# Kernel optimization log

Measured on AMD Instinct MI355X. Metric: run time of the kernel, lower is better.

Reference implementation:

```python
import jax, jax.numpy as jnp
import numpy as np

L = 5          # num_layer
D = 128        # emb_dim
F = 16         # raw node/edge feature dim
N = 50000      # nodes
E = 800000     # edges
BN_EPS = 1e-5


def _bn(z, g, b):
    # BatchNorm1d forward with batch statistics (training-mode math)
    m = z.mean(axis=0)
    v = z.var(axis=0)
    return (z - m) * jax.lax.rsqrt(v + BN_EPS) * g + b


def setup_inputs() -> dict:
    key = jax.random.key(0)
    ks = jax.random.split(key, 8)
    s = lambda *sh: 0.05  # weight scale
    return {
        "x": jax.random.normal(ks[0], (N, F), jnp.float32),
        "edge_index": jax.random.randint(ks[1], (2, E), 0, N, jnp.int32),
        "edge_attr": jax.random.normal(ks[2], (E, F), jnp.float32),
        "W_node": jax.random.normal(ks[3], (F, D), jnp.float32) * 0.05,
        "b_node": jnp.zeros((D,), jnp.float32),
        "We": jax.random.normal(ks[4], (L, F, D), jnp.float32) * 0.05,
        "be": jnp.zeros((L, D), jnp.float32),
        "eps_gin": jnp.zeros((L,), jnp.float32),
        "W1": jax.random.normal(ks[5], (L, D, 2 * D), jnp.float32) * 0.05,
        "b1": jnp.zeros((L, 2 * D), jnp.float32),
        "g1": jnp.ones((L, 2 * D), jnp.float32),
        "beta1": jnp.zeros((L, 2 * D), jnp.float32),
        "W2": jax.random.normal(ks[6], (L, 2 * D, D), jnp.float32) * 0.05,
        "b2": jnp.zeros((L, D), jnp.float32),
        "g_bn": jnp.ones((L, D), jnp.float32),
        "beta_bn": jnp.zeros((L, D), jnp.float32),
    }


def reference(x, edge_index, edge_attr, W_node, b_node, We, be, eps_gin,
              W1, b1, g1, beta1, W2, b2, g_bn, beta_bn):
    src, dst = edge_index[0], edge_index[1]
    n = x.shape[0]
    h = x @ W_node + b_node                       # node encoder: [N, D]
    for l in range(L):
        e = edge_attr @ We[l] + be[l]             # edge encoder: [E, D]
        msg = jax.nn.relu(h[src] + e)             # gather + message
        agg = jax.ops.segment_sum(msg, dst, num_segments=n)  # scatter-add
        z = (1.0 + eps_gin[l]) * h + agg
        z = _bn(z @ W1[l] + b1[l], g1[l], beta1[l])  # GIN MLP hidden
        z = jax.nn.relu(z)
        z = z @ W2[l] + b2[l]                     # GIN MLP out: [N, D]
        z = _bn(z, g_bn[l], beta_bn[l])           # per-layer BatchNorm
        if l < L - 1:
            z = jax.nn.relu(z)                    # dropout is identity (p=0)
        h = z + h                                 # residual
    return h                                      # JK = 'last'
```

## Files before the change

kernel.cpp:

```cpp
#include <hip/hip_runtime.h>
#include <hip/hip_bf16.h>

#define NN 50000
#define EE 800000
#define DD 128
#define FF 16
#define LL 5
#define NB 782

typedef __attribute__((ext_vector_type(8))) short bf16x8;
typedef __attribute__((ext_vector_type(4))) float f32x4;

__device__ __forceinline__ unsigned short f2bf(float f) {
    union { float f; unsigned int u; } v; v.f = f;
    unsigned int u = v.u;
    unsigned int r = (u + 0x7fffu + ((u >> 16) & 1u)) >> 16;
    return (unsigned short)r;
}
__device__ __forceinline__ float bf2f(unsigned short s) {
    union { unsigned int u; float f; } v; v.u = ((unsigned int)s) << 16;
    return v.f;
}
#define BFLO(u) __uint_as_float((unsigned int)(u) << 16)
#define BFHI(u) __uint_as_float((unsigned int)(u) & 0xffff0000u)

__global__ void k_node_enc(const float* __restrict__ x, const float* __restrict__ Wn,
                           const float* __restrict__ bn, float* __restrict__ h,
                           unsigned short* __restrict__ h_bf)
{
    const int t = blockIdx.x * 256 + threadIdx.x;
    const int i = t >> 7, d = t & 127;
    const float4* x4 = (const float4*)(x + (size_t)i * 16);
    float4 a0 = x4[0], a1 = x4[1], a2 = x4[2], a3 = x4[3];
    float acc = bn[d];
    acc += a0.x*Wn[0*128+d] + a0.y*Wn[1*128+d] + a0.z*Wn[2*128+d] + a0.w*Wn[3*128+d];
    acc += a1.x*Wn[4*128+d] + a1.y*Wn[5*128+d] + a1.z*Wn[6*128+d] + a1.w*Wn[7*128+d];
    acc += a2.x*Wn[8*128+d] + a2.y*Wn[9*128+d] + a2.z*Wn[10*128+d] + a2.w*Wn[11*128+d];
    acc += a3.x*Wn[12*128+d] + a3.y*Wn[13*128+d] + a3.z*Wn[14*128+d] + a3.w*Wn[15*128+d];
    h[t] = acc;
    h_bf[t] = f2bf(acc);
}

__global__ void k_count(const int* __restrict__ ei, int* __restrict__ counts)
{
    const int e = blockIdx.x * 256 + threadIdx.x;
    atomicAdd(&counts[ei[EE + e]], 1);
}

__global__ __launch_bounds__(1024) void k_scan(int* __restrict__ counts, int* __restrict__ row_ptr)
{
    __shared__ int wsum[16];
    __shared__ int carry;
    const int tid = threadIdx.x, lane = tid & 63, w = tid >> 6;
    if (tid == 0) carry = 0;
    __syncthreads();
    for (int base = 0; base < NN; base += 1024) {
        const int i = base + tid;
        const int v = (i < NN) ? counts[i] : 0;
        int x = v;
        #pragma unroll
        for (int off = 1; off < 64; off <<= 1) {
            const int t = __shfl_up(x, off);
            if (lane >= off) x += t;
        }
        if (lane == 63) wsum[w] = x;
        __syncthreads();
        int woff = 0, total = 0;
        #pragma unroll
        for (int j = 0; j < 16; ++j) { const int s = wsum[j]; total += s; if (j < w) woff += s; }
        const int ex = carry + woff + x - v;
        if (i < NN) { row_ptr[i] = ex; counts[i] = ex; }
        __syncthreads();
        if (tid == 0) carry += total;
        __syncthreads();
    }
    if (tid == 0) row_ptr[NN] = carry;
}

__global__ void k_fill(const int* __restrict__ ei, const float* __restrict__ ea,
                       int* __restrict__ cursor, int* __restrict__ src_perm,
                       unsigned short* __restrict__ ea_bf)
{
    const int e = blockIdx.x * 256 + threadIdx.x;
    const int dst = ei[EE + e];
    const int p = atomicAdd(&cursor[dst], 1);
    src_perm[p] = ei[e];
    const float4* s4 = (const float4*)(ea + (size_t)e * 16);
    const float4 a0 = s4[0], a1 = s4[1], a2 = s4[2], a3 = s4[3];
    union { bf16x8 v; unsigned short u[8]; } o0, o1;
    o0.u[0]=f2bf(a0.x); o0.u[1]=f2bf(a0.y); o0.u[2]=f2bf(a0.z); o0.u[3]=f2bf(a0.w);
    o0.u[4]=f2bf(a1.x); o0.u[5]=f2bf(a1.y); o0.u[6]=f2bf(a1.z); o0.u[7]=f2bf(a1.w);
    o1.u[0]=f2bf(a2.x); o1.u[1]=f2bf(a2.y); o1.u[2]=f2bf(a2.z); o1.u[3]=f2bf(a2.w);
    o1.u[4]=f2bf(a3.x); o1.u[5]=f2bf(a3.y); o1.u[6]=f2bf(a3.z); o1.u[7]=f2bf(a3.w);
    bf16x8* dp = (bf16x8*)(ea_bf + (size_t)p * 16);
    dp[0] = o0.v; dp[1] = o1.v;
}

__global__ void k_pack(const float* __restrict__ W1, const float* __restrict__ W2,
                       unsigned short* __restrict__ Wp1, unsigned short* __restrict__ Wp2)
{
    int t = blockIdx.x * 256 + threadIdx.x;
    const int total = LL * 32768;
    if (t < total) {
        const int l = t >> 15, r = t & 32767;
        const int j = r & 7, lane = (r >> 3) & 63, kt = (r >> 9) & 3, nt = r >> 11;
        const int k = kt * 32 + (lane >> 4) * 8 + j;
        const int n = nt * 16 + (lane & 15);
        Wp1[t] = f2bf(W1[(size_t)l * 32768 + k * 256 + n]);
    } else {
        t -= total;
        const int l = t >> 15, r = t & 32767;
        const int j = r & 7, lane = (r >> 3) & 63, kt = (r >> 9) & 7, nt = r >> 12;
        const int k = kt * 32 + (lane >> 4) * 8 + j;
        const int n = nt * 16 + (lane & 15);
        Wp2[t] = f2bf(W2[(size_t)l * 32768 + k * 128 + n]);
    }
}

__global__ __launch_bounds__(256) void k_agg(
    const unsigned short* __restrict__ h_bf, const unsigned short* __restrict__ ea_bf,
    const float* __restrict__ We_l, const float* __restrict__ be_l,
    const float* __restrict__ eps_gin, const int l,
    const int* __restrict__ row_ptr, const int* __restrict__ src_perm,
    unsigned short* __restrict__ z_bf)
{
    const int wv = threadIdx.x >> 6;
    const int v  = blockIdx.x * 4 + wv;
    const int lane = threadIdx.x & 63;
    const int c2 = lane * 2;
    float2 w[16];
    #pragma unroll
    for (int f = 0; f < 16; ++f) w[f] = *(const float2*)(We_l + f * 128 + c2);
    const float2 bed = *(const float2*)(be_l + c2);
    const float epsv = 1.0f + eps_gin[l];
    const int kbeg = __builtin_amdgcn_readfirstlane(row_ptr[v]);
    const int kend = __builtin_amdgcn_readfirstlane(row_ptr[v + 1]);
    float2 acc0 = {0.f,0.f}, acc1 = {0.f,0.f}, acc2 = {0.f,0.f}, acc3 = {0.f,0.f};

#define EDGE_DOT(EA, EB, HQ, OUT) do {                                      \
        float ex_ = bed.x, ey_ = bed.y, a_;                                 \
        a_ = BFLO(EA.x); ex_ += a_*w[0].x;  ey_ += a_*w[0].y;               \
        a_ = BFHI(EA.x); ex_ += a_*w[1].x;  ey_ += a_*w[1].y;               \
        a_ = BFLO(EA.y); ex_ += a_*w[2].x;  ey_ += a_*w[2].y;               \
        a_ = BFHI(EA.y); ex_ += a_*w[3].x;  ey_ += a_*w[3].y;               \
        a_ = BFLO(EA.z); ex_ += a_*w[4].x;  ey_ += a_*w[4].y;               \
        a_ = BFHI(EA.z); ex_ += a_*w[5].x;  ey_ += a_*w[5].y;               \
        a_ = BFLO(EA.w); ex_ += a_*w[6].x;  ey_ += a_*w[6].y;               \
        a_ = BFHI(EA.w); ex_ += a_*w[7].x;  ey_ += a_*w[7].y;               \
        a_ = BFLO(EB.x); ex_ += a_*w[8].x;  ey_ += a_*w[8].y;               \
        a_ = BFHI(EB.x); ex_ += a_*w[9].x;  ey_ += a_*w[9].y;               \
        a_ = BFLO(EB.y); ex_ += a_*w[10].x; ey_ += a_*w[10].y;              \
        a_ = BFHI(EB.y); ex_ += a_*w[11].x; ey_ += a_*w[11].y;              \
        a_ = BFLO(EB.z); ex_ += a_*w[12].x; ey_ += a_*w[12].y;              \
        a_ = BFHI(EB.z); ex_ += a_*w[13].x; ey_ += a_*w[13].y;              \
        a_ = BFLO(EB.w); ex_ += a_*w[14].x; ey_ += a_*w[14].y;              \
        a_ = BFHI(EB.w); ex_ += a_*w[15].x; ey_ += a_*w[15].y;              \
        const float mx_ = BFLO(HQ) + ex_, my_ = BFHI(HQ) + ey_;             \
        OUT.x += mx_ > 0.f ? mx_ : 0.f;                                     \
        OUT.y += my_ > 0.f ? my_ : 0.f;                                     \
    } while (0)

    uint4 ce0, ce1, ce2, ce3, ce4, ce5, ce6, ce7;
    unsigned int ch0, ch1, ch2, ch3;
    int vs0, vs1, vs2, vs3;

    int k = kbeg;
    if (k < kend) {
        const int a0 = __builtin_amdgcn_readfirstlane(src_perm[k]);
        const int a1 = __builtin_amdgcn_readfirstlane(src_perm[k + 1]);
        const int a2 = __builtin_amdgcn_readfirstlane(src_perm[k + 2]);
        const int a3 = __builtin_amdgcn_readfirstlane(src_perm[k + 3]);
        ch0 = *(const unsigned int*)(h_bf + (size_t)a0 * 128 + c2);
        ch1 = *(const unsigned int*)(h_bf + (size_t)a1 * 128 + c2);
        ch2 = *(const unsigned int*)(h_bf + (size_t)a2 * 128 + c2);
        ch3 = *(const unsigned int*)(h_bf + (size_t)a3 * 128 + c2);
        const uint4* ep = (const uint4*)(ea_bf + (size_t)k * 16);
        ce0 = ep[0]; ce1 = ep[1]; ce2 = ep[2]; ce3 = ep[3];
        ce4 = ep[4]; ce5 = ep[5]; ce6 = ep[6]; ce7 = ep[7];
        vs0 = src_perm[k + 4]; vs1 = src_perm[k + 5];
        vs2 = src_perm[k + 6]; vs3 = src_perm[k + 7];
    }
    for (; k < kend; k += 4) {
        const int fs0 = src_perm[k + 8],  fs1 = src_perm[k + 9];
        const int fs2 = src_perm[k + 10], fs3 = src_perm[k + 11];
        const int b0 = __builtin_amdgcn_readfirstlane(vs0);
        const int b1 = __builtin_amdgcn_readfirstlane(vs1);
        const int b2 = __builtin_amdgcn_readfirstlane(vs2);
        const int b3 = __builtin_amdgcn_readfirstlane(vs3);
        const unsigned int nh0 = *(const unsigned int*)(h_bf + (size_t)b0 * 128 + c2);
        const unsigned int nh1 = *(const unsigned int*)(h_bf + (size_t)b1 * 128 + c2);
        const unsigned int nh2 = *(const unsigned int*)(h_bf + (size_t)b2 * 128 + c2);
        const unsigned int nh3 = *(const unsigned int*)(h_bf + (size_t)b3 * 128 + c2);
        const uint4* np_ = (const uint4*)(ea_bf + (size_t)(k + 4) * 16);
        const uint4 ne0 = np_[0], ne1 = np_[1], ne2 = np_[2], ne3 = np_[3];
        const uint4 ne4 = np_[4], ne5 = np_[5], ne6 = np_[6], ne7 = np_[7];
        __builtin_amdgcn_sched_barrier(0);
        EDGE_DOT(ce0, ce1, ch0, acc0);
        if (k + 1 < kend) EDGE_DOT(ce2, ce3, ch1, acc1);
        if (k + 2 < kend) EDGE_DOT(ce4, ce5, ch2, acc2);
        if (k + 3 < kend) EDGE_DOT(ce6, ce7, ch3, acc3);
        ce0=ne0; ce1=ne1; ce2=ne2; ce3=ne3; ce4=ne4; ce5=ne5; ce6=ne6; ce7=ne7;
        ch0=nh0; ch1=nh1; ch2=nh2; ch3=nh3;
        vs0=fs0; vs1=fs1; vs2=fs2; vs3=fs3;
    }
#undef EDGE_DOT
    const unsigned int hv = *(const unsigned int*)(h_bf + (size_t)v * 128 + c2);
    const float zx = epsv * BFLO(hv) + ((acc0.x + acc1.x) + (acc2.x + acc3.x));
    const float zy = epsv * BFHI(hv) + ((acc0.y + acc1.y) + (acc2.y + acc3.y));
    const unsigned int zp = (unsigned int)f2bf(zx) | ((unsigned int)f2bf(zy) << 16);
    *(unsigned int*)(z_bf + (size_t)v * 128 + c2) = zp;
}

__global__ __launch_bounds__(256) void k_gemmB(
    const unsigned short* __restrict__ z_bf,
    const unsigned short* __restrict__ Wp,
    unsigned short* __restrict__ t_bf,
    float* __restrict__ ps1, float* __restrict__ pq1)
{
    const int tid = threadIdx.x;
    const int w = tid >> 6, l6 = tid & 63, m = l6 & 15, quad = l6 >> 4;
    const int r0 = blockIdx.x * 64;
    const bf16x8* Wv = (const bf16x8*)Wp;
    bf16x8 b[4][4];
    #pragma unroll
    for (int ct = 0; ct < 4; ++ct)
        #pragma unroll
        for (int kt = 0; kt < 4; ++kt)
            b[ct][kt] = Wv[((w * 4 + ct) * 4 + kt) * 64 + l6];

    const bf16x8 zero8 = {0,0,0,0,0,0,0,0};
    const f32x4 z4 = {0.f, 0.f, 0.f, 0.f};
    float rs_[4] = {0.f,0.f,0.f,0.f}, rq_[4] = {0.f,0.f,0.f,0.f};

    bf16x8 a[4], an[4];
    {
        const int row = r0 + m;
        #pragma unroll
        for (int kt = 0; kt < 4; ++kt)
            a[kt] = (row < NN) ? *(const bf16x8*)(z_bf + (size_t)row * 128 + kt * 32 + quad * 8) : zero8;
    }
    #pragma unroll
    for (int rt = 0; rt < 4; ++rt) {
        if (rt < 3) {
            const int row = r0 + (rt + 1) * 16 + m;
            #pragma unroll
            for (int kt = 0; kt < 4; ++kt)
                an[kt] = (row < NN) ? *(const bf16x8*)(z_bf + (size_t)row * 128 + kt * 32 + quad * 8) : zero8;
        }
        f32x4 acc[4] = {z4, z4, z4, z4};
        #pragma unroll
        for (int kt = 0; kt < 4; ++kt)
            #pragma unroll
            for (int ct = 0; ct < 4; ++ct)
                acc[ct] = __builtin_amdgcn_mfma_f32_16x16x32_bf16(a[kt], b[ct][kt], acc[ct], 0, 0, 0);
        const int rowb = r0 + rt * 16 + quad * 4;
        #pragma unroll
        for (int ct = 0; ct < 4; ++ct) {
            const int col = w * 64 + ct * 16 + m;
            #pragma unroll
            for (int r = 0; r < 4; ++r) {
                const float val = acc[ct][r];
                if (rowb + r < NN) t_bf[(size_t)(rowb + r) * 256 + col] = f2bf(val);
                rs_[ct] += val; rq_[ct] += val * val;
            }
        }
        #pragma unroll
        for (int kt = 0; kt < 4; ++kt) a[kt] = an[kt];
    }
    #pragma unroll
    for (int ct = 0; ct < 4; ++ct) {
        float ss = rs_[ct], sq = rq_[ct];
        ss += __shfl_xor(ss, 16); ss += __shfl_xor(ss, 32);
        sq += __shfl_xor(sq, 16); sq += __shfl_xor(sq, 32);
        if (quad == 0) {
            const int col = w * 64 + ct * 16 + m;
            atomicAdd(&ps1[col], ss);
            atomicAdd(&pq1[col], sq);
        }
    }
}

__global__ __launch_bounds__(256) void k_gemmD(
    const unsigned short* __restrict__ t_bf,
    const float* __restrict__ ps1, const float* __restrict__ pq1,
    const float* __restrict__ g1, const float* __restrict__ be1,
    const unsigned short* __restrict__ Wp,
    unsigned short* __restrict__ vb,
    float* __restrict__ ps2, float* __restrict__ pq2)
{
    __shared__ __align__(16) unsigned short us[64 * 264];
    __shared__ __align__(16) float scf[256], shf[256];
    const int tid = threadIdx.x;
    {
        const float mean = ps1[tid] * (1.0f / NN);
        const float var  = pq1[tid] * (1.0f / NN) - mean * mean;
        const float sc = g1[tid] * rsqrtf(var + 1e-5f);
        scf[tid] = sc;
        shf[tid] = be1[tid] - mean * sc;
    }
    __syncthreads();
    const int r0 = blockIdx.x * 64;
    {
        const int rb = tid >> 5, c0 = (tid & 31) * 8;
        const float4 s0 = *(const float4*)(scf + c0), s1 = *(const float4*)(scf + c0 + 4);
        const float4 b0 = *(const float4*)(shf + c0), b1 = *(const float4*)(shf + c0 + 4);
        const bf16x8 zero = {0,0,0,0,0,0,0,0};
        #pragma unroll
        for (int rr = 0; rr < 8; ++rr) {
            const int row = rr * 8 + rb, g = r0 + row;
            union { bf16x8 v; unsigned short u[8]; } in, o;
            if (g < NN) {
                in.v = *(const bf16x8*)(t_bf + (size_t)g * 256 + c0);
                float xv;
                xv = bf2f(in.u[0])*s0.x + b0.x; o.u[0] = f2bf(xv > 0.f ? xv : 0.f);
                xv = bf2f(in.u[1])*s0.y + b0.y; o.u[1] = f2bf(xv > 0.f ? xv : 0.f);
                xv = bf2f(in.u[2])*s0.z + b0.z; o.u[2] = f2bf(xv > 0.f ? xv : 0.f);
                xv = bf2f(in.u[3])*s0.w + b0.w; o.u[3] = f2bf(xv > 0.f ? xv : 0.f);
                xv = bf2f(in.u[4])*s1.x + b1.x; o.u[4] = f2bf(xv > 0.f ? xv : 0.f);
                xv = bf2f(in.u[5])*s1.y + b1.y; o.u[5] = f2bf(xv > 0.f ? xv : 0.f);
                xv = bf2f(in.u[6])*s1.z + b1.z; o.u[6] = f2bf(xv > 0.f ? xv : 0.f);
                xv = bf2f(in.u[7])*s1.w + b1.w; o.u[7] = f2bf(xv > 0.f ? xv : 0.f);
            } else {
                o.v = zero;
            }
            *(bf16x8*)(&us[row * 264 + c0]) = o.v;
        }
    }
    __syncthreads();
    const int w = tid >> 6, l6 = tid & 63, m = l6 & 15, quad = l6 >> 4;
    const bf16x8* Wv = (const bf16x8*)Wp;
    bf16x8 b[2][8];
    #pragma unroll
    for (int ct = 0; ct < 2; ++ct)
        #pragma unroll
        for (int kt = 0; kt < 8; ++kt)
            b[ct][kt] = Wv[((w * 2 + ct) * 8 + kt) * 64 + l6];

    const f32x4 z4 = {0.f, 0.f, 0.f, 0.f};
    float rs_[2] = {0.f,0.f}, rq_[2] = {0.f,0.f};
    #pragma unroll
    for (int rt = 0; rt < 4; ++rt) {
        bf16x8 a[8];
        #pragma unroll
        for (int kt = 0; kt < 8; ++kt)
            a[kt] = *(const bf16x8*)(&us[(rt * 16 + m) * 264 + kt * 32 + quad * 8]);
        f32x4 acc[2] = {z4, z4};
        #pragma unroll
        for (int kt = 0; kt < 8; ++kt)
            #pragma unroll
            for (int ct = 0; ct < 2; ++ct)
                acc[ct] = __builtin_amdgcn_mfma_f32_16x16x32_bf16(a[kt], b[ct][kt], acc[ct], 0, 0, 0);
        const int rowb = r0 + rt * 16 + quad * 4;
        #pragma unroll
        for (int ct = 0; ct < 2; ++ct) {
            const int col = w * 32 + ct * 16 + m;
            #pragma unroll
            for (int r = 0; r < 4; ++r) {
                const float val = acc[ct][r];
                if (rowb + r < NN) vb[(size_t)(rowb + r) * 128 + col] = f2bf(val);
                rs_[ct] += val; rq_[ct] += val * val;
            }
        }
    }
    #pragma unroll
    for (int ct = 0; ct < 2; ++ct) {
        float ss = rs_[ct], sq = rq_[ct];
        ss += __shfl_xor(ss, 16); ss += __shfl_xor(ss, 32);
        sq += __shfl_xor(sq, 16); sq += __shfl_xor(sq, 32);
        if (quad == 0) {
            const int col = w * 32 + ct * 16 + m;
            atomicAdd(&ps2[col], ss);
            atomicAdd(&pq2[col], sq);
        }
    }
}

__global__ void k_fin(const unsigned short* __restrict__ vb,
                      const float* __restrict__ ps2, const float* __restrict__ pq2,
                      const float* __restrict__ g2, const float* __restrict__ be2,
                      float* __restrict__ h, unsigned short* __restrict__ h_bf,
                      const int do_relu)
{
    __shared__ __align__(16) float scf[128], shf[128];
    const int tid = threadIdx.x;
    if (tid < 128) {
        const float mean = ps2[tid] * (1.0f / NN);
        const float var  = pq2[tid] * (1.0f / NN) - mean * mean;
        const float sc = g2[tid] * rsqrtf(var + 1e-5f);
        scf[tid] = sc;
        shf[tid] = be2[tid] - mean * sc;
    }
    __syncthreads();
    const int t = blockIdx.x * 256 + tid;
    const int base = t * 8;
    const int c = base & 127;
    union { bf16x8 v; unsigned short u[8]; } in, ob;
    in.v = *(const bf16x8*)(vb + base);
    const float4 s0 = *(const float4*)(scf + c), s1 = *(const float4*)(scf + c + 4);
    const float4 b0 = *(const float4*)(shf + c), b1 = *(const float4*)(shf + c + 4);
    float4 h0 = *(const float4*)(h + base), h1 = *(const float4*)(h + base + 4);
    float z;
    z = bf2f(in.u[0])*s0.x + b0.x; if (do_relu) z = z > 0.f ? z : 0.f; h0.x += z;
    z = bf2f(in.u[1])*s0.y + b0.y; if (do_relu) z = z > 0.f ? z : 0.f; h0.y += z;
    z = bf2f(in.u[2])*s0.z + b0.z; if (do_relu) z = z > 0.f ? z : 0.f; h0.z += z;
    z = bf2f(in.u[3])*s0.w + b0.w; if (do_relu) z = z > 0.f ? z : 0.f; h0.w += z;
    z = bf2f(in.u[4])*s1.x + b1.x; if (do_relu) z = z > 0.f ? z : 0.f; h1.x += z;
    z = bf2f(in.u[5])*s1.y + b1.y; if (do_relu) z = z > 0.f ? z : 0.f; h1.y += z;
    z = bf2f(in.u[6])*s1.z + b1.z; if (do_relu) z = z > 0.f ? z : 0.f; h1.z += z;
    z = bf2f(in.u[7])*s1.w + b1.w; if (do_relu) z = z > 0.f ? z : 0.f; h1.w += z;
    *(float4*)(h + base) = h0;
    *(float4*)(h + base + 4) = h1;
    ob.u[0]=f2bf(h0.x); ob.u[1]=f2bf(h0.y); ob.u[2]=f2bf(h0.z); ob.u[3]=f2bf(h0.w);
    ob.u[4]=f2bf(h1.x); ob.u[5]=f2bf(h1.y); ob.u[6]=f2bf(h1.z); ob.u[7]=f2bf(h1.w);
    *(bf16x8*)(h_bf + base) = ob.v;
}

extern "C" void kernel_launch(void* const* d_in, const int* in_sizes, int n_in,
                              void* d_out, int out_size, void* d_ws, size_t ws_size,
                              hipStream_t stream)
{
    const float* x       = (const float*)d_in[0];
    const int*   ei      = (const int*)  d_in[1];
    const float* ea      = (const float*)d_in[2];
    const float* W_node  = (const float*)d_in[3];
    const float* b_node  = (const float*)d_in[4];
    const float* We      = (const float*)d_in[5];
    const float* be      = (const float*)d_in[6];
    const float* eps_gin = (const float*)d_in[7];
    const float* W1      = (const float*)d_in[8];
    const float* g1      = (const float*)d_in[10];
    const float* beta1   = (const float*)d_in[11];
    const float* W2      = (const float*)d_in[12];
    const float* g_bn    = (const float*)d_in[14];
    const float* beta_bn = (const float*)d_in[15];

    float* h = (float*)d_out;

    char* W = (char*)d_ws;
    int*   counts   = (int*)  (W + 0);
    int*   row_ptr  = (int*)  (W + 200000);
    float* stats    = (float*)(W + 400064);
    float* ps1 = stats, *pq1 = stats + 256, *ps2 = stats + 512, *pq2 = stats + 640;
    int*   src_perm = (int*)  (W + 403136);
    unsigned short* ea_bf = (unsigned short*)(W + 3603200);
    unsigned short* Wp1   = (unsigned short*)(W + 29203712);
    unsigned short* Wp2   = (unsigned short*)(W + 29531392);
    unsigned short* z_bf  = (unsigned short*)(W + 29859072);
    unsigned short* t_bf  = (unsigned short*)(W + 42659072);
    unsigned short* h_bf  = (unsigned short*)(W + 68259072);
    unsigned short* vb    = z_bf;

    (void)hipMemsetAsync(counts, 0, 200000, stream);
    (void)hipMemsetAsync(src_perm + EE, 0, 64, stream);

    k_node_enc<<<dim3(NN * DD / 256), dim3(256), 0, stream>>>(x, W_node, b_node, h, h_bf);
    k_count<<<dim3(EE / 256), dim3(256), 0, stream>>>(ei, counts);
    k_scan<<<dim3(1), dim3(1024), 0, stream>>>(counts, row_ptr);
    k_fill<<<dim3(EE / 256), dim3(256), 0, stream>>>(ei, ea, counts, src_perm, ea_bf);
    k_pack<<<dim3(2 * LL * 32768 / 256), dim3(256), 0, stream>>>(W1, W2, Wp1, Wp2);

    for (int l = 0; l < LL; ++l) {
        (void)hipMemsetAsync(stats, 0, 3072, stream);
        k_agg<<<dim3(NN / 4), dim3(256), 0, stream>>>(
            h_bf, ea_bf, We + (size_t)l * FF * DD, be + (size_t)l * DD,
            eps_gin, l, row_ptr, src_perm, z_bf);
        k_gemmB<<<dim3(NB), dim3(256), 0, stream>>>(
            z_bf, Wp1 + (size_t)l * 32768, t_bf, ps1, pq1);
        k_gemmD<<<dim3(NB), dim3(256), 0, stream>>>(
            t_bf, ps1, pq1, g1 + (size_t)l * 256, beta1 + (size_t)l * 256,
            Wp2 + (size_t)l * 32768, vb, ps2, pq2);
        k_fin<<<dim3(NN * DD / 8 / 256), dim3(256), 0, stream>>>(
            vb, ps2, pq2, g_bn + (size_t)l * 128, beta_bn + (size_t)l * 128,
            h, h_bf, (l < LL - 1) ? 1 : 0);
    }
}
```

Measured before the change: 927.3 us.

## Use fp16 edge attrs with fdot2, halve GEMM row tiles, fold stats memset

Edge attributes are now stored as fp16 pairs, and the edge-encoder dot product uses packed fdot2 instructions in place of 32 scalar FMAs per edge. This cuts ALU work in the aggregation kernel, at the cost of fp16 range and precision on weights and attributes. Separately, both GEMM kernels now process 32 rows per block, doubling the grid to improve load balance across CUs. The per-layer stats memset is removed and the zeroing is folded into block 0 of k_agg.

```diff
diff --git a/kernel.cpp b/kernel.cpp
--- a/kernel.cpp
+++ b/kernel.cpp
@@ -6,10 +6,11 @@
 #define DD 128
 #define FF 16
 #define LL 5
-#define NB 782
+#define NB32 1563
 
 typedef __attribute__((ext_vector_type(8))) short bf16x8;
 typedef __attribute__((ext_vector_type(4))) float f32x4;
+typedef __attribute__((ext_vector_type(2))) _Float16 half2_t;
 
 __device__ __forceinline__ unsigned short f2bf(float f) {
     union { float f; unsigned int u; } v; v.f = f;
@@ -23,6 +24,22 @@
 }
 #define BFLO(u) __uint_as_float((unsigned int)(u) << 16)
 #define BFHI(u) __uint_as_float((unsigned int)(u) & 0xffff0000u)
+
+__device__ __forceinline__ half2_t u2h2(unsigned int u) {
+    union { unsigned int u; half2_t h; } v; v.u = u; return v.h;
+}
+__device__ __forceinline__ unsigned int pkh2(float a, float b) {
+    union { half2_t h; unsigned int u; } v;
+    v.h[0] = (_Float16)a; v.h[1] = (_Float16)b; return v.u;
+}
+#if __has_builtin(__builtin_amdgcn_fdot2)
+#define FDOT2(A, B, C) __builtin_amdgcn_fdot2((A), (B), (C), false)
+#else
+__device__ __forceinline__ float fdot2_fb(half2_t a, half2_t b, float c) {
+    return (float)a[0] * (float)b[0] + (float)a[1] * (float)b[1] + c;
+}
+#define FDOT2(A, B, C) fdot2_fb((A), (B), (C))
+#endif
 
 __global__ void k_node_enc(const float* __restrict__ x, const float* __restrict__ Wn,
                            const float* __restrict__ bn, float* __restrict__ h,
@@ -79,7 +96,7 @@
 
 __global__ void k_fill(const int* __restrict__ ei, const float* __restrict__ ea,
                        int* __restrict__ cursor, int* __restrict__ src_perm,
-                       unsigned short* __restrict__ ea_bf)
+                       unsigned int* __restrict__ ea_h)
 {
     const int e = blockIdx.x * 256 + threadIdx.x;
     const int dst = ei[EE + e];
@@ -87,13 +104,13 @@
     src_perm[p] = ei[e];
     const float4* s4 = (const float4*)(ea + (size_t)e * 16);
     const float4 a0 = s4[0], a1 = s4[1], a2 = s4[2], a3 = s4[3];
-    union { bf16x8 v; unsigned short u[8]; } o0, o1;
-    o0.u[0]=f2bf(a0.x); o0.u[1]=f2bf(a0.y); o0.u[2]=f2bf(a0.z); o0.u[3]=f2bf(a0.w);
-    o0.u[4]=f2bf(a1.x); o0.u[5]=f2bf(a1.y); o0.u[6]=f2bf(a1.z); o0.u[7]=f2bf(a1.w);
-    o1.u[0]=f2bf(a2.x); o1.u[1]=f2bf(a2.y); o1.u[2]=f2bf(a2.z); o1.u[3]=f2bf(a2.w);
-    o1.u[4]=f2bf(a3.x); o1.u[5]=f2bf(a3.y); o1.u[6]=f2bf(a3.z); o1.u[7]=f2bf(a3.w);
-    bf16x8* dp = (bf16x8*)(ea_bf + (size_t)p * 16);
-    dp[0] = o0.v; dp[1] = o1.v;
+    union { uint4 v[2]; unsigned int u[8]; } o;
+    o.u[0] = pkh2(a0.x, a0.y); o.u[1] = pkh2(a0.z, a0.w);
+    o.u[2] = pkh2(a1.x, a1.y); o.u[3] = pkh2(a1.z, a1.w);
+    o.u[4] = pkh2(a2.x, a2.y); o.u[5] = pkh2(a2.z, a2.w);
+    o.u[6] = pkh2(a3.x, a3.y); o.u[7] = pkh2(a3.z, a3.w);
+    uint4* dp = (uint4*)(ea_h + (size_t)p * 8);
+    dp[0] = o.v[0]; dp[1] = o.v[1];
 }
 
 __global__ void k_pack(const float* __restrict__ W1, const float* __restrict__ W2,
@@ -118,19 +135,27 @@
 }
 
 __global__ __launch_bounds__(256) void k_agg(
-    const unsigned short* __restrict__ h_bf, const unsigned short* __restrict__ ea_bf,
+    const unsigned short* __restrict__ h_bf, const unsigned int* __restrict__ ea_h,
     const float* __restrict__ We_l, const float* __restrict__ be_l,
     const float* __restrict__ eps_gin, const int l,
     const int* __restrict__ row_ptr, const int* __restrict__ src_perm,
-    unsigned short* __restrict__ z_bf)
-{
+    unsigned short* __restrict__ z_bf, float* __restrict__ stats)
+{
+    if (blockIdx.x == 0) {
+        stats[threadIdx.x] = 0.f;
+        stats[threadIdx.x + 256] = 0.f;
+        stats[threadIdx.x + 512] = 0.f;
+    }
     const int wv = threadIdx.x >> 6;
     const int v  = blockIdx.x * 4 + wv;
     const int lane = threadIdx.x & 63;
     const int c2 = lane * 2;
-    float2 w[16];
-    #pragma unroll
-    for (int f = 0; f < 16; ++f) w[f] = *(const float2*)(We_l + f * 128 + c2);
+    half2_t wx[8], wy[8];
+    #pragma unroll
+    for (int j = 0; j < 8; ++j) {
+        wx[j] = u2h2(pkh2(We_l[(2*j) * 128 + c2],     We_l[(2*j+1) * 128 + c2]));
+        wy[j] = u2h2(pkh2(We_l[(2*j) * 128 + c2 + 1], We_l[(2*j+1) * 128 + c2 + 1]));
+    }
     const float2 bed = *(const float2*)(be_l + c2);
     const float epsv = 1.0f + eps_gin[l];
     const int kbeg = __builtin_amdgcn_readfirstlane(row_ptr[v]);
@@ -138,23 +163,19 @@
     float2 acc0 = {0.f,0.f}, acc1 = {0.f,0.f}, acc2 = {0.f,0.f}, acc3 = {0.f,0.f};
 
 #define EDGE_DOT(EA, EB, HQ, OUT) do {                                      \
-        float ex_ = bed.x, ey_ = bed.y, a_;                                 \
-        a_ = BFLO(EA.x); ex_ += a_*w[0].x;  ey_ += a_*w[0].y;               \
-        a_ = BFHI(EA.x); ex_ += a_*w[1].x;  ey_ += a_*w[1].y;               \
-        a_ = BFLO(EA.y); ex_ += a_*w[2].x;  ey_ += a_*w[2].y;               \
-        a_ = BFHI(EA.y); ex_ += a_*w[3].x;  ey_ += a_*w[3].y;               \
-        a_ = BFLO(EA.z); ex_ += a_*w[4].x;  ey_ += a_*w[4].y;               \
-        a_ = BFHI(EA.z); ex_ += a_*w[5].x;  ey_ += a_*w[5].y;               \
-        a_ = BFLO(EA.w); ex_ += a_*w[6].x;  ey_ += a_*w[6].y;               \
-        a_ = BFHI(EA.w); ex_ += a_*w[7].x;  ey_ += a_*w[7].y;               \
-        a_ = BFLO(EB.x); ex_ += a_*w[8].x;  ey_ += a_*w[8].y;               \
-        a_ = BFHI(EB.x); ex_ += a_*w[9].x;  ey_ += a_*w[9].y;               \
-        a_ = BFLO(EB.y); ex_ += a_*w[10].x; ey_ += a_*w[10].y;              \
-        a_ = BFHI(EB.y); ex_ += a_*w[11].x; ey_ += a_*w[11].y;              \
-        a_ = BFLO(EB.z); ex_ += a_*w[12].x; ey_ += a_*w[12].y;              \
-        a_ = BFHI(EB.z); ex_ += a_*w[13].x; ey_ += a_*w[13].y;              \
-        a_ = BFLO(EB.w); ex_ += a_*w[14].x; ey_ += a_*w[14].y;              \
-        a_ = BFHI(EB.w); ex_ += a_*w[15].x; ey_ += a_*w[15].y;              \
+        float ex_ = bed.x, ey_ = bed.y;                                     \
+        const half2_t q0_ = u2h2(EA.x), q1_ = u2h2(EA.y);                   \
+        const half2_t q2_ = u2h2(EA.z), q3_ = u2h2(EA.w);                   \
+        const half2_t q4_ = u2h2(EB.x), q5_ = u2h2(EB.y);                   \
+        const half2_t q6_ = u2h2(EB.z), q7_ = u2h2(EB.w);                   \
+        ex_ = FDOT2(q0_, wx[0], ex_); ey_ = FDOT2(q0_, wy[0], ey_);         \
+        ex_ = FDOT2(q1_, wx[1], ex_); ey_ = FDOT2(q1_, wy[1], ey_);         \
+        ex_ = FDOT2(q2_, wx[2], ex_); ey_ = FDOT2(q2_, wy[2], ey_);         \
+        ex_ = FDOT2(q3_, wx[3], ex_); ey_ = FDOT2(q3_, wy[3], ey_);         \
+        ex_ = FDOT2(q4_, wx[4], ex_); ey_ = FDOT2(q4_, wy[4], ey_);         \
+        ex_ = FDOT2(q5_, wx[5], ex_); ey_ = FDOT2(q5_, wy[5], ey_);         \
+        ex_ = FDOT2(q6_, wx[6], ex_); ey_ = FDOT2(q6_, wy[6], ey_);         \
+        ex_ = FDOT2(q7_, wx[7], ex_); ey_ = FDOT2(q7_, wy[7], ey_);         \
         const float mx_ = BFLO(HQ) + ex_, my_ = BFHI(HQ) + ey_;             \
         OUT.x += mx_ > 0.f ? mx_ : 0.f;                                     \
         OUT.y += my_ > 0.f ? my_ : 0.f;                                     \
@@ -174,7 +195,7 @@
         ch1 = *(const unsigned int*)(h_bf + (size_t)a1 * 128 + c2);
         ch2 = *(const unsigned int*)(h_bf + (size_t)a2 * 128 + c2);
         ch3 = *(const unsigned int*)(h_bf + (size_t)a3 * 128 + c2);
-        const uint4* ep = (const uint4*)(ea_bf + (size_t)k * 16);
+        const uint4* ep = (const uint4*)(ea_h + (size_t)k * 8);
         ce0 = ep[0]; ce1 = ep[1]; ce2 = ep[2]; ce3 = ep[3];
         ce4 = ep[4]; ce5 = ep[5]; ce6 = ep[6]; ce7 = ep[7];
         vs0 = src_perm[k + 4]; vs1 = src_perm[k + 5];
@@ -191,7 +212,7 @@
         const unsigned int nh1 = *(const unsigned int*)(h_bf + (size_t)b1 * 128 + c2);
         const unsigned int nh2 = *(const unsigned int*)(h_bf + (size_t)b2 * 128 + c2);
         const unsigned int nh3 = *(const unsigned int*)(h_bf + (size_t)b3 * 128 + c2);
-        const uint4* np_ = (const uint4*)(ea_bf + (size_t)(k + 4) * 16);
+        const uint4* np_ = (const uint4*)(ea_h + (size_t)(k + 4) * 8);
         const uint4 ne0 = np_[0], ne1 = np_[1], ne2 = np_[2], ne3 = np_[3];
         const uint4 ne4 = np_[4], ne5 = np_[5], ne6 = np_[6], ne7 = np_[7];
         __builtin_amdgcn_sched_barrier(0);
@@ -219,7 +240,7 @@
 {
     const int tid = threadIdx.x;
     const int w = tid >> 6, l6 = tid & 63, m = l6 & 15, quad = l6 >> 4;
-    const int r0 = blockIdx.x * 64;
+    const int r0 = blockIdx.x * 32;
     const bf16x8* Wv = (const bf16x8*)Wp;
     bf16x8 b[4][4];
     #pragma unroll
@@ -240,9 +261,9 @@
             a[kt] = (row < NN) ? *(const bf16x8*)(z_bf + (size_t)row * 128 + kt * 32 + quad * 8) : zero8;
     }
     #pragma unroll
-    for (int rt = 0; rt < 4; ++rt) {
-        if (rt < 3) {
-            const int row = r0 + (rt + 1) * 16 + m;
+    for (int rt = 0; rt < 2; ++rt) {
+        if (rt < 1) {
+            const int row = r0 + 16 + m;
             #pragma unroll
             for (int kt = 0; kt < 4; ++kt)
                 an[kt] = (row < NN) ? *(const bf16x8*)(z_bf + (size_t)row * 128 + kt * 32 + quad * 8) : zero8;
@@ -288,7 +309,7 @@
     unsigned short* __restrict__ vb,
     float* __restrict__ ps2, float* __restrict__ pq2)
 {
-    __shared__ __align__(16) unsigned short us[64 * 264];
+    __shared__ __align__(16) unsigned short us[32 * 264];
     __shared__ __align__(16) float scf[256], shf[256];
     const int tid = threadIdx.x;
     {
@@ -299,14 +320,14 @@
         shf[tid] = be1[tid] - mean * sc;
     }
     __syncthreads();
-    const int r0 = blockIdx.x * 64;
+    const int r0 = blockIdx.x * 32;
     {
         const int rb = tid >> 5, c0 = (tid & 31) * 8;
         const float4 s0 = *(const float4*)(scf + c0), s1 = *(const float4*)(scf + c0 + 4);
         const float4 b0 = *(const float4*)(shf + c0), b1 = *(const float4*)(shf + c0 + 4);
         const bf16x8 zero = {0,0,0,0,0,0,0,0};
         #pragma unroll
-        for (int rr = 0; rr < 8; ++rr) {
+        for (int rr = 0; rr < 4; ++rr) {
             const int row = rr * 8 + rb, g = r0 + row;
             union { bf16x8 v; unsigned short u[8]; } in, o;
             if (g < NN) {
@@ -339,7 +360,7 @@
     const f32x4 z4 = {0.f, 0.f, 0.f, 0.f};
     float rs_[2] = {0.f,0.f}, rq_[2] = {0.f,0.f};
     #pragma unroll
-    for (int rt = 0; rt < 4; ++rt) {
+    for (int rt = 0; rt < 2; ++rt) {
         bf16x8 a[8];
         #pragma unroll
         for (int kt = 0; kt < 8; ++kt)
@@ -442,13 +463,13 @@
     float* stats    = (float*)(W + 400064);
     float* ps1 = stats, *pq1 = stats + 256, *ps2 = stats + 512, *pq2 = stats + 640;
     int*   src_perm = (int*)  (W + 403136);
-    unsigned short* ea_bf = (unsigned short*)(W + 3603200);
-    unsigned short* Wp1   = (unsigned short*)(W + 29203712);
-    unsigned short* Wp2   = (unsigned short*)(W + 29531392);
-    unsigned short* z_bf  = (unsigned short*)(W + 29859072);
-    unsigned short* t_bf  = (unsigned short*)(W + 42659072);
-    unsigned short* h_bf  = (unsigned short*)(W + 68259072);
-    unsigned short* vb    = z_bf;
+    unsigned int* ea_h   = (unsigned int*)(W + 3603200);
+    unsigned short* Wp1  = (unsigned short*)(W + 29203712);
+    unsigned short* Wp2  = (unsigned short*)(W + 29531392);
+    unsigned short* z_bf = (unsigned short*)(W + 29859072);
+    unsigned short* t_bf = (unsigned short*)(W + 42659072);
+    unsigned short* h_bf = (unsigned short*)(W + 68259072);
+    unsigned short* vb   = z_bf;
 
     (void)hipMemsetAsync(counts, 0, 200000, stream);
     (void)hipMemsetAsync(src_perm + EE, 0, 64, stream);
@@ -456,17 +477,16 @@
     k_node_enc<<<dim3(NN * DD / 256), dim3(256), 0, stream>>>(x, W_node, b_node, h, h_bf);
     k_count<<<dim3(EE / 256), dim3(256), 0, stream>>>(ei, counts);
     k_scan<<<dim3(1), dim3(1024), 0, stream>>>(counts, row_ptr);
-    k_fill<<<dim3(EE / 256), dim3(256), 0, stream>>>(ei, ea, counts, src_perm, ea_bf);
+    k_fill<<<dim3(EE / 256), dim3(256), 0, stream>>>(ei, ea, counts, src_perm, ea_h);
     k_pack<<<dim3(2 * LL * 32768 / 256), dim3(256), 0, stream>>>(W1, W2, Wp1, Wp2);
 
     for (int l = 0; l < LL; ++l) {
-        (void)hipMemsetAsync(stats, 0, 3072, stream);
         k_agg<<<dim3(NN / 4), dim3(256), 0, stream>>>(
-            h_bf, ea_bf, We + (size_t)l * FF * DD, be + (size_t)l * DD,
-            eps_gin, l, row_ptr, src_perm, z_bf);
-        k_gemmB<<<dim3(NB), dim3(256), 0, stream>>>(
+            h_bf, ea_h, We + (size_t)l * FF * DD, be + (size_t)l * DD,
+            eps_gin, l, row_ptr, src_perm, z_bf, stats);
+        k_gemmB<<<dim3(NB32), dim3(256), 0, stream>>>(
             z_bf, Wp1 + (size_t)l * 32768, t_bf, ps1, pq1);
-        k_gemmD<<<dim3(NB), dim3(256), 0, stream>>>(
+        k_gemmD<<<dim3(NB32), dim3(256), 0, stream>>>(
             t_bf, ps1, pq1, g1 + (size_t)l * 256, beta1 + (size_t)l * 256,
             Wp2 + (size_t)l * 32768, vb, ps2, pq2);
         k_fin<<<dim3(NN * DD / 8 / 256), dim3(256), 0, stream>>>(
```

Result: slower. 1.098 ms (+18.4%).
